# Optimization experiments

Hardware: AMD Instinct MI355X
Metric: run time of the kernel (lower is better)

## Reference

```python
import jax, jax.numpy as jnp
import numpy as np

THRESHOLD = 0.5
NEG_POS_RATIO = 3
ALPHA = 1.0
BETA = 1.0
IGNORE_INDEX = 255

B, P, C, O = 16, 16384, 21, 16
H = W = 256


def cxcy_to_xy(c):
    return jnp.concatenate([c[..., :2] - c[..., 2:] / 2, c[..., :2] + c[..., 2:] / 2], axis=-1)


def xy_to_cxcy(xy):
    return jnp.concatenate([(xy[..., :2] + xy[..., 2:]) / 2, xy[..., 2:] - xy[..., :2]], axis=-1)


def cxcy_to_gcxgcy(cxcy, priors_cxcy):
    return jnp.concatenate([
        (cxcy[..., :2] - priors_cxcy[..., :2]) / (priors_cxcy[..., 2:] / 10.0),
        jnp.log(cxcy[..., 2:] / priors_cxcy[..., 2:]) * 5.0,
    ], axis=-1)


def jaccard(set1, set2):
    # set1 [O,4] xy, set2 [P,4] xy -> IoU [O,P]
    lo = jnp.maximum(set1[:, None, :2], set2[None, :, :2])
    hi = jnp.minimum(set1[:, None, 2:], set2[None, :, 2:])
    wh = jnp.clip(hi - lo, 0.0)
    inter = wh[..., 0] * wh[..., 1]
    a1 = (set1[:, 2] - set1[:, 0]) * (set1[:, 3] - set1[:, 1])
    a2 = (set2[:, 2] - set2[:, 0]) * (set2[:, 3] - set2[:, 1])
    return inter / (a1[:, None] + a2[None, :] - inter)


def setup_inputs() -> dict:
    key = jax.random.key(0)
    ks = jax.random.split(key, 8)
    predicted_locs = jax.random.normal(ks[0], (B, P, 4), dtype=jnp.float32)
    predicted_scores = jax.random.normal(ks[1], (B, P, C), dtype=jnp.float32)
    predicted_masks = jax.random.normal(ks[2], (B, C, H, W), dtype=jnp.float32)
    x1y1 = jax.random.uniform(ks[3], (B, O, 2), dtype=jnp.float32) * 0.8
    wh = jax.random.uniform(ks[4], (B, O, 2), dtype=jnp.float32) * 0.19 + 0.01
    boxes = jnp.concatenate([x1y1, x1y1 + wh], axis=-1)  # valid xy boxes
    pc = jax.random.uniform(ks[5], (P, 2), dtype=jnp.float32) * 0.9 + 0.05
    pwh = jax.random.uniform(ks[6], (P, 2), dtype=jnp.float32) * 0.28 + 0.02
    priors_cxcy = jnp.concatenate([pc, pwh], axis=-1)
    labels = jax.random.randint(ks[7], (B, O), 1, C)  # object labels, never background
    masks = jax.random.randint(jax.random.fold_in(key, 99), (B, 1, H, W), 0, C)
    return {
        'predicted_locs': predicted_locs,
        'predicted_scores': predicted_scores,
        'predicted_masks': predicted_masks,
        'boxes': boxes,
        'priors_cxcy': priors_cxcy,
        'labels': labels,
        'masks': masks,
    }


def _assign(bx, lb, priors_cxcy, priors_xy):
    # bx [O,4] xy, lb [O] int -> true_locs [P,4], true_classes [P]
    ov = jaccard(bx, priors_xy)  # [O,P]
    overlap_for_each_prior = ov.max(axis=0)       # [P]
    object_for_each_prior = ov.argmax(axis=0)     # [P]
    prior_for_each_object = ov.argmax(axis=1)     # [O]
    # guarantee every object is matched to its best prior
    object_for_each_prior = object_for_each_prior.at[prior_for_each_object].set(jnp.arange(O))
    overlap_for_each_prior = overlap_for_each_prior.at[prior_for_each_object].set(1.0)
    label_for_each_prior = lb[object_for_each_prior]
    label_for_each_prior = jnp.where(overlap_for_each_prior < THRESHOLD, 0, label_for_each_prior)
    true_locs = cxcy_to_gcxgcy(xy_to_cxcy(bx[object_for_each_prior]), priors_cxcy)
    return true_locs, label_for_each_prior


def reference(predicted_locs, predicted_scores, predicted_masks, boxes, priors_cxcy, labels, masks):
    priors_xy = cxcy_to_xy(priors_cxcy)
    true_locs, true_classes = jax.vmap(_assign, in_axes=(0, 0, None, None))(
        boxes, labels, priors_cxcy, priors_xy)  # [B,P,4], [B,P]

    pos = true_classes != 0                      # [B,P]
    pos_f = pos.astype(predicted_locs.dtype)
    n_pos = pos.sum(axis=1)                      # [B]

    # localization: L1Loss (mean over positive prior elements)
    diff = jnp.abs(predicted_locs - true_locs)
    loc_loss = (diff * pos_f[..., None]).sum() / jnp.maximum(pos_f.sum() * 4.0, 1.0)

    # confidence: CE per prior + hard negative mining
    logp = jax.nn.log_softmax(predicted_scores, axis=-1)            # [B,P,C]
    ce = -jnp.take_along_axis(logp, true_classes[..., None], axis=-1)[..., 0]  # [B,P]
    ce_pos_sum = (ce * pos_f).sum()
    ce_neg = jnp.where(pos, 0.0, ce)
    ce_neg_sorted = -jnp.sort(-ce_neg, axis=1)                      # descending
    ranks = jnp.arange(P)[None, :]
    hard = (ranks < (NEG_POS_RATIO * n_pos)[:, None]).astype(ce.dtype)
    ce_hardneg_sum = (ce_neg_sorted * hard).sum()
    conf_loss = (ce_hardneg_sum + ce_pos_sum) / n_pos.sum().astype(ce.dtype)

    # mask loss: cross_entropy2d, sum reduction then / (H*W) / B
    tgt = masks[:, 0]                                                # [B,H,W]
    valid = (tgt != IGNORE_INDEX)
    t = jnp.where(valid, tgt, 0)
    logp_m = jax.nn.log_softmax(predicted_masks, axis=1)             # [B,C,H,W]
    ce_m = -jnp.take_along_axis(logp_m, t[:, None], axis=1)[:, 0]    # [B,H,W]
    mask_loss = (ce_m * valid.astype(ce_m.dtype)).sum() / (H * W) / B

    return conf_loss + ALPHA * loc_loss + BETA * mask_loss
```

## Files before the change

kernel.cpp:

```cpp
#include <hip/hip_runtime.h>
#include <cstdint>
#include <cstddef>

#define Bn 16
#define Pn 16384
#define Cn 21
#define On 16
#define HWn 65536
#define THRESH 0.5f


__device__ __forceinline__ float waveReduceSum(float v) {
  for (int off = 32; off > 0; off >>= 1) v += __shfl_down(v, off, 64);
  return v;
}
__device__ __forceinline__ int waveReduceSumI(int v) {
  for (int off = 32; off > 0; off >>= 1) v += __shfl_down(v, off, 64);
  return v;
}

__global__ __launch_bounds__(256) void k_phase1(
    const float* __restrict__ boxes, const float* __restrict__ priors,
    unsigned long long* __restrict__ partials, float* __restrict__ accum,
    int* __restrict__ n_pos, int* __restrict__ n_pos_total,
    int* __restrict__ done_cnt) {
  const int b = blockIdx.x >> 6;
  const int blk = blockIdx.x & 63;
  const int p = (blk << 8) + threadIdx.x;
  if (blockIdx.x == 0) {
    if (threadIdx.x < 4) accum[threadIdx.x] = 0.f;
    if (threadIdx.x < On) n_pos[threadIdx.x] = 0;
    if (threadIdx.x == 32) *n_pos_total = 0;
    if (threadIdx.x == 33) *done_cnt = 0;
  }
  __shared__ float4 sbox[On];
  __shared__ float sarea[On];
  __shared__ unsigned long long skey[On];
  if (threadIdx.x < On) {
    float4 bx = ((const float4*)boxes)[b * On + threadIdx.x];
    sbox[threadIdx.x] = bx;
    sarea[threadIdx.x] = (bx.z - bx.x) * (bx.w - bx.y);
    skey[threadIdx.x] = 0ULL;
  }
  __syncthreads();
  float4 pr = ((const float4*)priors)[p];
  const float px1 = pr.x - 0.5f * pr.z, py1 = pr.y - 0.5f * pr.w;
  const float px2 = pr.x + 0.5f * pr.z, py2 = pr.y + 0.5f * pr.w;
  const float parea = pr.z * pr.w;
  const int lane = threadIdx.x & 63;
#pragma unroll
  for (int o = 0; o < On; ++o) {
    float4 bx = sbox[o];
    float ix = fmaxf(fminf(px2, bx.z) - fmaxf(px1, bx.x), 0.f);
    float iy = fmaxf(fminf(py2, bx.w) - fmaxf(py1, bx.y), 0.f);
    float inter = ix * iy;
    float iou = inter / (sarea[o] + parea - inter);
    unsigned long long key = ((unsigned long long)__float_as_uint(iou) << 32)
                           | (unsigned long long)(0xFFFFFFFFu - (unsigned)p);
    for (int off = 32; off > 0; off >>= 1) {
      unsigned long long other = __shfl_xor(key, off, 64);
      key = key > other ? key : other;
    }
    if (lane == 0) atomicMax(&skey[o], key);
  }
  __syncthreads();
  if (threadIdx.x < On)
    partials[((size_t)blockIdx.x) * On + threadIdx.x] = skey[threadIdx.x];
}

__global__ __launch_bounds__(256) void k_fused(
    const float* __restrict__ plocs, const float* __restrict__ pscores,
    const float* __restrict__ pm, const float* __restrict__ boxes,
    const float* __restrict__ priors, const int* __restrict__ labels,
    const int* __restrict__ msk, const unsigned long long* __restrict__ partials,
    float* __restrict__ ce_neg, float* __restrict__ accum,
    int* __restrict__ n_pos, int* __restrict__ n_pos_total) {
  __shared__ float ssc[256 * Cn];
  __shared__ float4 sbox[On];
  __shared__ float sarea[On];
  __shared__ int slab[On];
  __shared__ int spfo[On];
  __shared__ unsigned long long skey[On];
  __shared__ float sr1[4], sr2[4];
  __shared__ int sri[4];
  const int lane = threadIdx.x & 63, wave = threadIdx.x >> 6;

  if (blockIdx.x < 1024) {
    const int idx4 = blockIdx.x * 256 + threadIdx.x;
    const int b = idx4 >> 14;
    const int pix = (idx4 & 16383) << 2;
    int4 t4 = ((const int4*)msk)[idx4];
    const bool v0 = (t4.x != 255), v1 = (t4.y != 255), v2 = (t4.z != 255), v3 = (t4.w != 255);
    const int c0 = v0 ? t4.x : 0, c1 = v1 ? t4.y : 0, c2 = v2 ? t4.z : 0, c3 = v3 ? t4.w : 0;
    const float* base = pm + (size_t)b * Cn * HWn + pix;
    float s0 = 0.f, s1 = 0.f, s2 = 0.f, s3 = 0.f;
    float x0 = 0.f, x1 = 0.f, x2 = 0.f, x3 = 0.f;
#pragma unroll
    for (int c = 0; c < Cn; ++c) {
      float4 v = *((const float4*)(base + (size_t)c * HWn));
      s0 += __expf(v.x); s1 += __expf(v.y); s2 += __expf(v.z); s3 += __expf(v.w);
      if (c == c0) x0 = v.x;
      if (c == c1) x1 = v.y;
      if (c == c2) x2 = v.z;
      if (c == c3) x3 = v.w;
    }
    float contrib = (v0 ? (__logf(s0) - x0) : 0.f) + (v1 ? (__logf(s1) - x1) : 0.f) +
                    (v2 ? (__logf(s2) - x2) : 0.f) + (v3 ? (__logf(s3) - x3) : 0.f);
    float r = waveReduceSum(contrib);
    if (lane == 0) sr1[wave] = r;
    __syncthreads();
    if (threadIdx.x == 0) atomicAdd(&accum[3], sr1[0] + sr1[1] + sr1[2] + sr1[3]);
    return;
  }

  const int ab = blockIdx.x - 1024;
  const int b = ab >> 6;
  const int p0 = (ab & 63) << 8;
  const int p = p0 + threadIdx.x;
  {
    const float4* src = (const float4*)(pscores + ((size_t)b * Pn + p0) * Cn);
    float4* dst = (float4*)ssc;
#pragma unroll
    for (int i = threadIdx.x; i < (256 * Cn) / 4; i += 256) dst[i] = src[i];
  }
  if (threadIdx.x < On) skey[threadIdx.x] = 0ULL;
  if (threadIdx.x < On) {
    float4 bx = ((const float4*)boxes)[b * On + threadIdx.x];
    sbox[threadIdx.x] = bx;
    sarea[threadIdx.x] = (bx.z - bx.x) * (bx.w - bx.y);
    slab[threadIdx.x] = labels[b * On + threadIdx.x];
  }
  __syncthreads();
  {
    const int o = threadIdx.x & 15, j = threadIdx.x >> 4;
    const unsigned long long* pp = partials + ((size_t)b * 64) * On;
    unsigned long long k = 0ULL;
#pragma unroll
    for (int t = 0; t < 4; ++t) {
      unsigned long long v = pp[(size_t)(j * 4 + t) * On + o];
      k = v > k ? v : k;
    }
    atomicMax(&skey[o], k);
  }
  __syncthreads();
  if (threadIdx.x < On)
    spfo[threadIdx.x] = (int)(0xFFFFFFFFu - (unsigned)(skey[threadIdx.x] & 0xFFFFFFFFULL));
  __syncthreads();

  float4 pr = ((const float4*)priors)[p];
  const float px1 = pr.x - 0.5f * pr.z, py1 = pr.y - 0.5f * pr.w;
  const float px2 = pr.x + 0.5f * pr.z, py2 = pr.y + 0.5f * pr.w;
  const float parea = pr.z * pr.w;
  float best = -1.f;
  int bobj = 0;
#pragma unroll
  for (int o = 0; o < On; ++o) {
    float4 bx = sbox[o];
    float ix = fmaxf(fminf(px2, bx.z) - fmaxf(px1, bx.x), 0.f);
    float iy = fmaxf(fminf(py2, bx.w) - fmaxf(py1, bx.y), 0.f);
    float inter = ix * iy;
    float iou = inter / (sarea[o] + parea - inter);
    if (iou > best) { best = iou; bobj = o; }
  }
#pragma unroll
  for (int o = 0; o < On; ++o) {
    if (spfo[o] == p) { bobj = o; best = 1.0f; }
  }
  const int lbl = (best < THRESH) ? 0 : slab[bobj];
  const bool pos = (lbl != 0);
  float locp = 0.f;
  if (pos) {
    float4 bx = sbox[bobj];
    float cx = 0.5f * (bx.x + bx.z), cy = 0.5f * (bx.y + bx.w);
    float w = bx.z - bx.x, h = bx.w - bx.y;
    float g0 = (cx - pr.x) / (pr.z * 0.1f);
    float g1 = (cy - pr.y) / (pr.w * 0.1f);
    float g2 = logf(w / pr.z) * 5.f;
    float g3 = logf(h / pr.w) * 5.f;
    float4 pl = ((const float4*)plocs)[b * Pn + p];
    locp = fabsf(pl.x - g0) + fabsf(pl.y - g1) + fabsf(pl.z - g2) + fabsf(pl.w - g3);
  }
  const float* my = ssc + threadIdx.x * Cn;
  float s = 0.f, xt = 0.f;
#pragma unroll
  for (int c = 0; c < Cn; ++c) {
    float v = my[c];
    s += __expf(v);
    if (c == lbl) xt = v;
  }
  float ce = __logf(s) - xt;
  ce_neg[b * Pn + p] = pos ? 0.f : ce;
  float cep = pos ? ce : 0.f;

  float r1 = waveReduceSum(locp);
  float r2 = waveReduceSum(cep);
  int ri = waveReduceSumI(pos ? 1 : 0);
  if (lane == 0) { sr1[wave] = r1; sr2[wave] = r2; sri[wave] = ri; }
  __syncthreads();
  if (threadIdx.x == 0) {
    atomicAdd(&accum[0], sr1[0] + sr1[1] + sr1[2] + sr1[3]);
    atomicAdd(&accum[1], sr2[0] + sr2[1] + sr2[2] + sr2[3]);
    int ai = sri[0] + sri[1] + sri[2] + sri[3];
    atomicAdd(&n_pos[b], ai);
    atomicAdd(n_pos_total, ai);
  }
}

__global__ __launch_bounds__(256) void k_hardneg_final(
    const float* __restrict__ ce_neg, const int* __restrict__ n_pos,
    float* __restrict__ accum, const int* __restrict__ n_pos_total,
    int* __restrict__ done_cnt, float* __restrict__ out) {
  const int b = blockIdx.x;
  unsigned rv[64];
#pragma unroll
  for (int i = 0; i < 64; ++i)
    rv[i] = __float_as_uint(ce_neg[b * Pn + i * 256 + threadIdx.x]);
  int K = 3 * n_pos[b];
  if (K > Pn) K = Pn;
  __shared__ int scnt[4];
  __shared__ float ssum[4];
  const int lane = threadIdx.x & 63, wave = threadIdx.x >> 6;
  unsigned lo = 0u, hi = 0x7F800000u;
  while (lo < hi) {
    unsigned mid = lo + ((hi - lo) >> 1);
    int c = 0;
#pragma unroll
    for (int i = 0; i < 64; ++i) c += (rv[i] > mid) ? 1 : 0;
    c = waveReduceSumI(c);
    if (lane == 0) scnt[wave] = c;
    __syncthreads();
    int total = scnt[0] + scnt[1] + scnt[2] + scnt[3];
    if (total < K) hi = mid; else lo = mid + 1;
    __syncthreads();
  }
  const float fv = __uint_as_float(lo);
  float s = 0.f;
  int c = 0;
#pragma unroll
  for (int i = 0; i < 64; ++i) {
    if (rv[i] > lo) { s += __uint_as_float(rv[i]); c++; }
  }
  s = waveReduceSum(s);
  c = waveReduceSumI(c);
  if (lane == 0) { ssum[wave] = s; scnt[wave] = c; }
  __syncthreads();
  if (threadIdx.x == 0) {
    float tots = ssum[0] + ssum[1] + ssum[2] + ssum[3];
    int totc = scnt[0] + scnt[1] + scnt[2] + scnt[3];
    atomicAdd(&accum[2], tots + (float)(K - totc) * fv);
    __threadfence();
    int prev = atomicAdd(done_cnt, 1);
    if (prev == Bn - 1) {
      float a0 = atomicAdd(&accum[0], 0.f);
      float a1 = atomicAdd(&accum[1], 0.f);
      float a2 = atomicAdd(&accum[2], 0.f);
      float a3 = atomicAdd(&accum[3], 0.f);
      float np = (float)(*n_pos_total);
      float conf = (a2 + a1) / np;
      float loc = a0 / fmaxf(np * 4.f, 1.f);
      float maskl = a3 / (float)HWn / (float)Bn;
      out[0] = conf + loc + maskl;
    }
  }
}

extern "C" void kernel_launch(void* const* d_in, const int* in_sizes, int n_in,
                              void* d_out, int out_size, void* d_ws, size_t ws_size,
                              hipStream_t stream) {
  const float* plocs   = (const float*)d_in[0];
  const float* pscores = (const float*)d_in[1];
  const float* pmasks  = (const float*)d_in[2];
  const float* boxes   = (const float*)d_in[3];
  const float* priors  = (const float*)d_in[4];
  const int*   labels  = (const int*)d_in[5];
  const int*   masks   = (const int*)d_in[6];

  char* ws = (char*)d_ws;
  float* accum = (float*)ws;
  int* n_pos = (int*)(ws + 64);
  int* n_pos_total = (int*)(ws + 128);
  int* done_cnt = (int*)(ws + 132);
  unsigned long long* partials = (unsigned long long*)(ws + 4096);
  float* ce_neg = (float*)(ws + 135168);

  k_phase1<<<Bn * 64, 256, 0, stream>>>(boxes, priors, partials, accum, n_pos,
                                        n_pos_total, done_cnt);
  k_fused<<<2048, 256, 0, stream>>>(plocs, pscores, pmasks, boxes, priors,
                                    labels, masks, partials, ce_neg, accum,
                                    n_pos, n_pos_total);
  k_hardneg_final<<<Bn, 256, 0, stream>>>(ce_neg, n_pos, accum, n_pos_total,
                                          done_cnt, (float*)d_out);
}
```

Baseline: 235.6 us.

## Stage mask and score loads through LDS via direct global-to-LDS DMA

The mask-loss blocks now use global_load_lds to copy 512 pixels × 21 channels into shared memory, then each thread handles two pixels, which doubles the number of mask blocks. The score-loading path also replaces its register round-trip with direct global-to-LDS loads. The aim is more memory-level parallelism and less VGPR pressure on the bandwidth-bound mask read. The cost is a 43KB LDS footprint that may reduce occupancy, plus extra syncs and more launched blocks.

```diff
diff --git a/kernel.cpp b/kernel.cpp
--- a/kernel.cpp
+++ b/kernel.cpp
@@ -8,6 +8,11 @@
 #define On 16
 #define HWn 65536
 #define THRESH 0.5f
+
+#define GLOAD_LDS16(gp, lp)                                              \
+  __builtin_amdgcn_global_load_lds(                                      \
+      (const __attribute__((address_space(1))) void*)(gp),               \
+      (__attribute__((address_space(3))) void*)(lp), 16, 0, 0)
 
 
 __device__ __forceinline__ float waveReduceSum(float v) {
@@ -75,7 +80,7 @@
     const int* __restrict__ msk, const unsigned long long* __restrict__ partials,
     float* __restrict__ ce_neg, float* __restrict__ accum,
     int* __restrict__ n_pos, int* __restrict__ n_pos_total) {
-  __shared__ float ssc[256 * Cn];
+  __shared__ float slds[Cn * 512];
   __shared__ float4 sbox[On];
   __shared__ float sarea[On];
   __shared__ int slab[On];
@@ -85,27 +90,28 @@
   __shared__ int sri[4];
   const int lane = threadIdx.x & 63, wave = threadIdx.x >> 6;
 
-  if (blockIdx.x < 1024) {
-    const int idx4 = blockIdx.x * 256 + threadIdx.x;
-    const int b = idx4 >> 14;
-    const int pix = (idx4 & 16383) << 2;
-    int4 t4 = ((const int4*)msk)[idx4];
-    const bool v0 = (t4.x != 255), v1 = (t4.y != 255), v2 = (t4.z != 255), v3 = (t4.w != 255);
-    const int c0 = v0 ? t4.x : 0, c1 = v1 ? t4.y : 0, c2 = v2 ? t4.z : 0, c3 = v3 ? t4.w : 0;
-    const float* base = pm + (size_t)b * Cn * HWn + pix;
-    float s0 = 0.f, s1 = 0.f, s2 = 0.f, s3 = 0.f;
-    float x0 = 0.f, x1 = 0.f, x2 = 0.f, x3 = 0.f;
+  if (blockIdx.x < 2048) {
+    const int b = blockIdx.x >> 7;
+    const int pix0 = (blockIdx.x & 127) << 9;
+    const float* gbase = pm + (size_t)b * Cn * HWn + pix0;
+    for (int i = wave; i < 2 * Cn; i += 4) {
+      const int c = i >> 1, h = i & 1;
+      GLOAD_LDS16(gbase + (size_t)c * HWn + h * 256 + lane * 4,
+                  &slds[c * 512 + h * 256]);
+    }
+    int2 t2 = ((const int2*)(msk + (size_t)b * HWn + pix0))[threadIdx.x];
+    __syncthreads();
+    float s0 = 0.f, s1 = 0.f, x0 = 0.f, x1 = 0.f;
 #pragma unroll
     for (int c = 0; c < Cn; ++c) {
-      float4 v = *((const float4*)(base + (size_t)c * HWn));
-      s0 += __expf(v.x); s1 += __expf(v.y); s2 += __expf(v.z); s3 += __expf(v.w);
-      if (c == c0) x0 = v.x;
-      if (c == c1) x1 = v.y;
-      if (c == c2) x2 = v.z;
-      if (c == c3) x3 = v.w;
-    }
-    float contrib = (v0 ? (__logf(s0) - x0) : 0.f) + (v1 ? (__logf(s1) - x1) : 0.f) +
-                    (v2 ? (__logf(s2) - x2) : 0.f) + (v3 ? (__logf(s3) - x3) : 0.f);
+      float2 v = *(const float2*)&slds[c * 512 + 2 * threadIdx.x];
+      s0 += __expf(v.x);
+      s1 += __expf(v.y);
+      if (c == t2.x) x0 = v.x;
+      if (c == t2.y) x1 = v.y;
+    }
+    const bool v0 = (t2.x != 255), v1 = (t2.y != 255);
+    float contrib = (v0 ? (__logf(s0) - x0) : 0.f) + (v1 ? (__logf(s1) - x1) : 0.f);
     float r = waveReduceSum(contrib);
     if (lane == 0) sr1[wave] = r;
     __syncthreads();
@@ -113,15 +119,14 @@
     return;
   }
 
-  const int ab = blockIdx.x - 1024;
+  const int ab = blockIdx.x - 2048;
   const int b = ab >> 6;
   const int p0 = (ab & 63) << 8;
   const int p = p0 + threadIdx.x;
   {
-    const float4* src = (const float4*)(pscores + ((size_t)b * Pn + p0) * Cn);
-    float4* dst = (float4*)ssc;
-#pragma unroll
-    for (int i = threadIdx.x; i < (256 * Cn) / 4; i += 256) dst[i] = src[i];
+    const float* src = pscores + ((size_t)b * Pn + p0) * Cn;
+    for (int i = wave; i < Cn; i += 4)
+      GLOAD_LDS16(src + i * 256 + lane * 4, &slds[i * 256]);
   }
   if (threadIdx.x < On) skey[threadIdx.x] = 0ULL;
   if (threadIdx.x < On) {
@@ -180,7 +185,7 @@
     float4 pl = ((const float4*)plocs)[b * Pn + p];
     locp = fabsf(pl.x - g0) + fabsf(pl.y - g1) + fabsf(pl.z - g2) + fabsf(pl.w - g3);
   }
-  const float* my = ssc + threadIdx.x * Cn;
+  const float* my = slds + threadIdx.x * Cn;
   float s = 0.f, xt = 0.f;
 #pragma unroll
   for (int c = 0; c < Cn; ++c) {
@@ -285,7 +290,7 @@
 
   k_phase1<<<Bn * 64, 256, 0, stream>>>(boxes, priors, partials, accum, n_pos,
                                         n_pos_total, done_cnt);
-  k_fused<<<2048, 256, 0, stream>>>(plocs, pscores, pmasks, boxes, priors,
+  k_fused<<<3072, 256, 0, stream>>>(plocs, pscores, pmasks, boxes, priors,
                                     labels, masks, partials, ce_neg, accum,
                                     n_pos, n_pos_total);
   k_hardneg_final<<<Bn, 256, 0, stream>>>(ce_neg, n_pos, accum, n_pos_total,
```

After: 235.3 us. No clear change (-0.1%).
